# Kernel tuning notes

Hardware: AMD Instinct MI355X
Metric: run time of the kernel (lower is better)

## Reference

```python
import jax, jax.numpy as jnp
import numpy as np

B, L, D = 64, 8192, 64  # n*b, h*w, d_o

def setup_inputs() -> dict:
    key = jax.random.key(0)
    k1, k2, k3, k4 = jax.random.split(key, 4)
    return {
        "q": jax.random.normal(k1, (B, 1, D), dtype=jnp.float32),
        "kc": jax.random.normal(k2, (B, L, D), dtype=jnp.float32),
        "kd": jax.random.normal(k3, (B, L, D), dtype=jnp.float32),
        "v": jax.random.normal(k4, (B, L, D), dtype=jnp.float32),
        "tc": jnp.ones((), dtype=jnp.float32),  # temperature_c (learned scalar)
        "td": jnp.ones((), dtype=jnp.float32),  # temperature_d (learned scalar)
    }

def reference(q, kc, kd, v, tc, td):
    # Collect stage: single query gathers over all h*w positions.
    # attn_col_logit: [B, 1, L]
    attn_col_logit = jnp.einsum("bod,bld->bol", q, kc) / tc
    attn_col = jax.nn.softmax(attn_col_logit, axis=2)  # softmax over L
    # (dropout is identity in eval mode)
    attn = jnp.einsum("bol,bld->bod", attn_col, v)  # [B, 1, D]
    # Diffuse stage: sigmoid gate per position, outer-product broadcast.
    attn_dif = jax.nn.sigmoid(jnp.einsum("bld,bod->blo", kd, q) / td)  # [B, L, 1]
    output = attn_dif * attn  # broadcast [B,L,1] * [B,1,D] -> [B,L,D]
    return output, attn_col_logit.squeeze(1)  # ([B,L,D], [B,L])
```

## Files before the change

kernel.cpp:

```cpp
#include <hip/hip_runtime.h>
#include <math.h>

#define BB 64
#define LL 8192
#define DD 64
#define NC 16
#define CHUNK (LL / NC)

__global__ __launch_bounds__(512) void k_collect(
    const float* __restrict__ q, const float* __restrict__ kc,
    const float* __restrict__ v, const float* __restrict__ tc_p,
    float* __restrict__ out_logits, float* __restrict__ sws,
    float* __restrict__ pvws)
{
    __shared__ float qs[DD];
    __shared__ float lg[CHUNK];
    __shared__ float red[32 * DD];
    __shared__ float sred[32];

    const int tid = threadIdx.x;
    const int b = blockIdx.x / NC;
    const int c = blockIdx.x % NC;
    const int l0 = c * CHUNK;

    if (tid < DD) qs[tid] = q[b * DD + tid];
    __syncthreads();

    const float inv_tc = 1.0f / tc_p[0];
    const int j = tid & 15;
    const int g = tid >> 4;

    const float4 q4 = *(const float4*)&qs[j * 4];
    const float* kcb = kc + ((size_t)b * LL + l0) * DD;
    const float* vb  = v  + ((size_t)b * LL + l0) * DD;

    float s = 0.f;
    float4 acc = make_float4(0.f, 0.f, 0.f, 0.f);

    #pragma unroll
    for (int it = 0; it < CHUNK / 32; ++it) {
        const int l = it * 32 + g;
        const float4 k4 = *(const float4*)&kcb[(size_t)l * DD + j * 4];
        const float4 v4 = *(const float4*)&vb[(size_t)l * DD + j * 4];
        float d = k4.x * q4.x + k4.y * q4.y + k4.z * q4.z + k4.w * q4.w;
        d += __shfl_xor(d, 1);
        d += __shfl_xor(d, 2);
        d += __shfl_xor(d, 4);
        d += __shfl_xor(d, 8);
        const float logit = d * inv_tc;
        if (j == 0) lg[l] = logit;
        const float p = __expf(logit);
        s += p;
        acc.x += p * v4.x;
        acc.y += p * v4.y;
        acc.z += p * v4.z;
        acc.w += p * v4.w;
    }

    if (j == 0) sred[g] = s;
    *(float4*)&red[g * DD + j * 4] = acc;
    __syncthreads();

    out_logits[(size_t)b * LL + l0 + tid] = lg[tid];

    if (tid < DD) {
        float pv = 0.f;
        #pragma unroll
        for (int r = 0; r < 32; ++r) pv += red[r * DD + tid];
        pvws[((size_t)b * NC + c) * DD + tid] = pv;
    }
    if (tid == 0) {
        float ss = 0.f;
        #pragma unroll
        for (int r = 0; r < 32; ++r) ss += sred[r];
        sws[b * NC + c] = ss;
    }
}

__global__ __launch_bounds__(64) void k_reduce(
    const float* __restrict__ sws, const float* __restrict__ pvws,
    float* __restrict__ attn_ws)
{
    const int b = blockIdx.x;
    const int d = threadIdx.x;
    float S = 0.f, a = 0.f;
    #pragma unroll
    for (int c = 0; c < NC; ++c) {
        S += sws[b * NC + c];
        a += pvws[((size_t)b * NC + c) * DD + d];
    }
    attn_ws[b * DD + d] = a / S;
}

__global__ __launch_bounds__(256) void k_diffuse(
    const float* __restrict__ q, const float* __restrict__ kd,
    const float* __restrict__ td_p, const float* __restrict__ attn_ws,
    float* __restrict__ out)
{
    __shared__ float qs[DD];
    __shared__ float as[DD];
    const int tid = threadIdx.x;
    const int blocksPerB = LL / 64;
    const int b = blockIdx.x / blocksPerB;
    const int l0 = (blockIdx.x % blocksPerB) * 64;

    if (tid < DD) {
        qs[tid] = q[b * DD + tid];
        as[tid] = attn_ws[b * DD + tid];
    }
    __syncthreads();

    const float inv_td = 1.0f / td_p[0];
    const int j = tid & 15;
    const int g = tid >> 4;

    const float4 q4 = *(const float4*)&qs[j * 4];
    const float4 a4 = *(const float4*)&as[j * 4];

    const float* kdb = kd + ((size_t)b * LL + l0) * DD;
    float* ob = out + ((size_t)b * LL + l0) * DD;

    #pragma unroll
    for (int it = 0; it < 4; ++it) {
        const int l = it * 16 + g;
        const float4 k4 = *(const float4*)&kdb[(size_t)l * DD + j * 4];
        float d = k4.x * q4.x + k4.y * q4.y + k4.z * q4.z + k4.w * q4.w;
        d += __shfl_xor(d, 1);
        d += __shfl_xor(d, 2);
        d += __shfl_xor(d, 4);
        d += __shfl_xor(d, 8);
        const float gate = 1.0f / (1.0f + __expf(-d * inv_td));
        float4 o4;
        o4.x = gate * a4.x;
        o4.y = gate * a4.y;
        o4.z = gate * a4.z;
        o4.w = gate * a4.w;
        *(float4*)&ob[(size_t)l * DD + j * 4] = o4;
    }
}

extern "C" void kernel_launch(void* const* d_in, const int* in_sizes, int n_in,
                              void* d_out, int out_size, void* d_ws, size_t ws_size,
                              hipStream_t stream) {
    const float* q  = (const float*)d_in[0];
    const float* kc = (const float*)d_in[1];
    const float* kd = (const float*)d_in[2];
    const float* v  = (const float*)d_in[3];
    const float* tc = (const float*)d_in[4];
    const float* td = (const float*)d_in[5];

    float* out        = (float*)d_out;
    float* out_logits = out + (size_t)BB * LL * DD;

    float* ws   = (float*)d_ws;
    float* sws  = ws;
    float* pvws = sws + BB * NC;
    float* attn = pvws + (size_t)BB * NC * DD;

    k_collect<<<BB * NC, 512, 0, stream>>>(q, kc, v, tc, out_logits, sws, pvws);
    k_reduce<<<BB, DD, 0, stream>>>(sws, pvws, attn);
    k_diffuse<<<BB * (LL / 64), 256, 0, stream>>>(q, kd, td, attn, out);
}
```

Before: 116.3 us.

## Split collect into separate logit and PV kernels with finer-grained blocks

The fused collect kernel, which used 1024 blocks of 512 threads each streaming 512 rows of kc and v, is split into a logit kernel and a PV kernel. Each new kernel uses 8192 blocks of 256 threads over 64 rows, and the exp weights pass between them through a workspace buffer. The aim is more blocks in flight to keep the memory pipe busy. In exchange it adds a kernel launch, a round trip of the p values through memory, and a larger final reduction over 128 partials per batch.

```diff
diff --git a/kernel.cpp b/kernel.cpp
--- a/kernel.cpp
+++ b/kernel.cpp
@@ -4,24 +4,23 @@
 #define BB 64
 #define LL 8192
 #define DD 64
-#define NC 16
-#define CHUNK (LL / NC)
+#define BPB 128
+#define ROWS 64
 
-__global__ __launch_bounds__(512) void k_collect(
+__global__ __launch_bounds__(256) void k_logit(
     const float* __restrict__ q, const float* __restrict__ kc,
-    const float* __restrict__ v, const float* __restrict__ tc_p,
-    float* __restrict__ out_logits, float* __restrict__ sws,
-    float* __restrict__ pvws)
+    const float* __restrict__ tc_p, float* __restrict__ out_logits,
+    float* __restrict__ pws, float* __restrict__ sws)
 {
     __shared__ float qs[DD];
-    __shared__ float lg[CHUNK];
-    __shared__ float red[32 * DD];
-    __shared__ float sred[32];
+    __shared__ float lg[ROWS];
+    __shared__ float pp[ROWS];
+    __shared__ float sred[16];
 
     const int tid = threadIdx.x;
-    const int b = blockIdx.x / NC;
-    const int c = blockIdx.x % NC;
-    const int l0 = c * CHUNK;
+    const int b  = blockIdx.x >> 7;
+    const int cb = blockIdx.x & (BPB - 1);
+    const int l0 = cb * ROWS;
 
     if (tid < DD) qs[tid] = q[b * DD + tid];
     __syncthreads();
@@ -32,48 +31,73 @@
 
     const float4 q4 = *(const float4*)&qs[j * 4];
     const float* kcb = kc + ((size_t)b * LL + l0) * DD;
-    const float* vb  = v  + ((size_t)b * LL + l0) * DD;
 
     float s = 0.f;
-    float4 acc = make_float4(0.f, 0.f, 0.f, 0.f);
-
     #pragma unroll
-    for (int it = 0; it < CHUNK / 32; ++it) {
-        const int l = it * 32 + g;
+    for (int it = 0; it < 4; ++it) {
+        const int l = it * 16 + g;
         const float4 k4 = *(const float4*)&kcb[(size_t)l * DD + j * 4];
-        const float4 v4 = *(const float4*)&vb[(size_t)l * DD + j * 4];
         float d = k4.x * q4.x + k4.y * q4.y + k4.z * q4.z + k4.w * q4.w;
         d += __shfl_xor(d, 1);
         d += __shfl_xor(d, 2);
         d += __shfl_xor(d, 4);
         d += __shfl_xor(d, 8);
         const float logit = d * inv_tc;
-        if (j == 0) lg[l] = logit;
         const float p = __expf(logit);
+        if (j == 0) { lg[l] = logit; pp[l] = p; }
         s += p;
+    }
+    if (j == 0) sred[g] = s;
+    __syncthreads();
+
+    if (tid < ROWS) {
+        out_logits[(size_t)b * LL + l0 + tid] = lg[tid];
+        pws[(size_t)b * LL + l0 + tid] = pp[tid];
+    }
+    if (tid == 0) {
+        float ss = 0.f;
+        #pragma unroll
+        for (int r = 0; r < 16; ++r) ss += sred[r];
+        sws[blockIdx.x] = ss;
+    }
+}
+
+__global__ __launch_bounds__(256) void k_pv(
+    const float* __restrict__ v, const float* __restrict__ pws,
+    float* __restrict__ pvws)
+{
+    __shared__ float red[16 * DD];
+
+    const int tid = threadIdx.x;
+    const int b  = blockIdx.x >> 7;
+    const int cb = blockIdx.x & (BPB - 1);
+    const int l0 = cb * ROWS;
+
+    const int j = tid & 15;
+    const int g = tid >> 4;
+
+    const float* vb = v + ((size_t)b * LL + l0) * DD;
+    const float* pb = pws + (size_t)b * LL + l0;
+
+    float4 acc = make_float4(0.f, 0.f, 0.f, 0.f);
+    #pragma unroll
+    for (int it = 0; it < 4; ++it) {
+        const int l = it * 16 + g;
+        const float4 v4 = *(const float4*)&vb[(size_t)l * DD + j * 4];
+        const float p = pb[l];
         acc.x += p * v4.x;
         acc.y += p * v4.y;
         acc.z += p * v4.z;
         acc.w += p * v4.w;
     }
-
-    if (j == 0) sred[g] = s;
     *(float4*)&red[g * DD + j * 4] = acc;
     __syncthreads();
-
-    out_logits[(size_t)b * LL + l0 + tid] = lg[tid];
 
     if (tid < DD) {
         float pv = 0.f;
         #pragma unroll
-        for (int r = 0; r < 32; ++r) pv += red[r * DD + tid];
-        pvws[((size_t)b * NC + c) * DD + tid] = pv;
-    }
-    if (tid == 0) {
-        float ss = 0.f;
-        #pragma unroll
-        for (int r = 0; r < 32; ++r) ss += sred[r];
-        sws[b * NC + c] = ss;
+        for (int r = 0; r < 16; ++r) pv += red[r * DD + tid];
+        pvws[(size_t)blockIdx.x * DD + tid] = pv;
     }
 }
 
@@ -84,10 +108,9 @@
     const int b = blockIdx.x;
     const int d = threadIdx.x;
     float S = 0.f, a = 0.f;
-    #pragma unroll
-    for (int c = 0; c < NC; ++c) {
-        S += sws[b * NC + c];
-        a += pvws[((size_t)b * NC + c) * DD + d];
+    for (int c = 0; c < BPB; ++c) {
+        S += sws[b * BPB + c];
+        a += pvws[((size_t)b * BPB + c) * DD + d];
     }
     attn_ws[b * DD + d] = a / S;
 }
@@ -100,9 +123,8 @@
     __shared__ float qs[DD];
     __shared__ float as[DD];
     const int tid = threadIdx.x;
-    const int blocksPerB = LL / 64;
-    const int b = blockIdx.x / blocksPerB;
-    const int l0 = (blockIdx.x % blocksPerB) * 64;
+    const int b  = blockIdx.x >> 7;
+    const int l0 = (blockIdx.x & (BPB - 1)) * ROWS;
 
     if (tid < DD) {
         qs[tid] = q[b * DD + tid];
@@ -153,11 +175,13 @@
     float* out_logits = out + (size_t)BB * LL * DD;
 
     float* ws   = (float*)d_ws;
-    float* sws  = ws;
-    float* pvws = sws + BB * NC;
-    float* attn = pvws + (size_t)BB * NC * DD;
+    float* pws  = ws;
+    float* sws  = pws + (size_t)BB * LL;
+    float* pvws = sws + BB * BPB;
+    float* attn = pvws + (size_t)BB * BPB * DD;
 
-    k_collect<<<BB * NC, 512, 0, stream>>>(q, kc, v, tc, out_logits, sws, pvws);
-    k_reduce<<<BB, DD, 0, stream>>>(sws, pvws, attn);
-    k_diffuse<<<BB * (LL / 64), 256, 0, stream>>>(q, kd, td, attn, out);
+    k_logit  <<<BB * BPB, 256, 0, stream>>>(q, kc, tc, out_logits, pws, sws);
+    k_pv     <<<BB * BPB, 256, 0, stream>>>(v, pws, pvws);
+    k_reduce <<<BB, DD, 0, stream>>>(sws, pvws, attn);
+    k_diffuse<<<BB * BPB, 256, 0, stream>>>(q, kd, td, attn, out);
 }
```

New measurement: 114.1 us. About the same (-1.9%).
